# Kernel tuning notes

Hardware: AMD Instinct MI355X
Metric: run time of the kernel (lower is better)

The kernel has to match this reference:

```python
import jax, jax.numpy as jnp
import numpy as np

# Static configuration (matches init_kwargs)
L = 3264          # seq_length
K = 12            # ktc=4 -> K=12
LOCC = 4          # ktc=4 -> Locc=4
S, B, A = 8, 64, 4  # streams (user/port pairs), batch, rx antennas
DELAY_MIN, DELAY_MAX = -10, 10


def _phasor(m):
    # m: integer shifts [S, B] -> exp(1j*2*pi*m*n/L) as [S, B, L]
    n = jnp.arange(L, dtype=jnp.int32)
    ang = (2.0 * np.pi / L) * ((m[..., None] * n) % L).astype(jnp.float32)
    return jax.lax.complex(jnp.cos(ang), jnp.sin(ang))


def _linear_interp(h_avg):
    # np.interp with uniform source grid orig[i] = (LOCC-1)/2 + i*LOCC, clamped at ends.
    # h_avg: [S, B, A, R] complex, R = L // LOCC -> [S, B, A, L]
    R = L // LOCC
    new = jnp.arange(L, dtype=jnp.float32)
    t = jnp.clip((new - (LOCC - 1) / 2.0) / LOCC, 0.0, float(R - 1))
    i0 = jnp.floor(t).astype(jnp.int32)
    i1 = jnp.minimum(i0 + 1, R - 1)
    frac = (t - i0).astype(jnp.float32)
    return h_avg[..., i0] * (1.0 - frac) + h_avg[..., i1] * frac


def reference(ls_real, ls_imag, cyclic_shifts, noise_powers):
    ls = jax.lax.complex(ls_real, ls_imag)                     # [S,B,A,L]
    ideal_peak = ((K - cyclic_shifts) % K) * (L // K)          # [S]

    # Stage 1: IFFT + timing-offset search (torch.no_grad in original)
    h_time = jnp.fft.ifft(ls, axis=-1)
    power = jax.lax.stop_gradient(jnp.sum(jnp.abs(h_time) ** 2, axis=2))  # [S,B,L]
    offs = jnp.arange(DELAY_MIN, DELAY_MAX + 1, dtype=jnp.int32)          # [21]
    cand_idx = (ideal_peak[:, None] + offs[None, :]) % L                   # [S,21]
    cand_idx = jnp.broadcast_to(cand_idx[:, None, :], (S, B, offs.shape[0]))
    cand_pow = jnp.take_along_axis(power, cand_idx, axis=-1)               # [S,B,21]
    t_off = offs[jnp.argmax(cand_pow, axis=-1)]                            # [S,B]
    m = t_off + ideal_peak[:, None]                                        # [S,B]
    ph_m = _phasor(m)        # [S,B,L]
    ph_T = _phasor(t_off)    # [S,B,L]

    # Stage 2: phasor shift, OCC demux, interpolation (inside no_grad in original)
    h_shift = ls * ph_m[:, :, None, :]
    h_avg = h_shift.reshape(S, B, A, L // LOCC, LOCC).mean(-1)             # [S,B,A,L/4]
    h_interp = jax.lax.stop_gradient(_linear_interp(h_avg))                # [S,B,A,L]

    # Stage 3: global residual against stream (0,0)'s LS estimate
    total_recon = jnp.sum(h_interp * jnp.conj(ph_m)[:, :, None, :], axis=0)  # [B,A,L]
    residual = ls[0] - total_recon                                           # [B,A,L]

    # Stage 4: apply residual, MMSE (identity: mmse_module=None), timing recovery
    h_wr = h_interp + residual[None, :, :, None, :].squeeze(3) if False else h_interp + residual[None] * ph_m[:, :, None, :]
    final = h_wr * jnp.conj(ph_T)[:, :, None, :]                             # [S,B,A,L]
    return jnp.stack([final.real, final.imag]).astype(jnp.float32)          # [2,S,B,A,L]


def setup_inputs() -> dict:
    key = jax.random.key(0)
    k1, k2, k3, k4 = jax.random.split(key, 4)
    return {
        "ls_real": jax.random.normal(k1, (S, B, A, L), dtype=jnp.float32),
        "ls_imag": jax.random.normal(k2, (S, B, A, L), dtype=jnp.float32),
        "cyclic_shifts": jax.random.randint(k3, (S,), 0, K, dtype=jnp.int32),
        "noise_powers": jax.random.uniform(k4, (B,), dtype=jnp.float32),
    }
```

## Files before the change

kernel.cpp:

```cpp
#include <hip/hip_runtime.h>

namespace {

constexpr int L = 3264;
constexpr int K = 12;
constexpr int S = 8;
constexpr int B = 64;
constexpr int A = 4;
constexpr int R = 816;
constexpr int NOFF = 21;
constexpr int PEAK_STEP = L / K;
constexpr float TWO_PI = 6.28318530717958647692f;
constexpr float CINV = TWO_PI / (float)L;
constexpr int NCHUNK = (L + 255) / 256;

__device__ __forceinline__ float2 cmul(float2 a, float2 b) {
    return make_float2(a.x * b.x - a.y * b.y, a.x * b.y + a.y * b.x);
}

__device__ __forceinline__ float rdl(float v, int d) {
    return __uint_as_float(__builtin_amdgcn_readlane(__float_as_uint(v), d));
}

__global__ __launch_bounds__(256)
void k_tables(const int* __restrict__ cs, float2* __restrict__ phT,
              float2* __restrict__ phI, float2* __restrict__ tw)
{
    const int g = blockIdx.x * 256 + threadIdx.x;
    if (g < NOFF * L) {
        const int t = g / L, l = g - t * L;
        int j = ((t - 10) * l) % L; if (j < 0) j += L;
        float sv, cv; __sincosf(CINV * (float)j, &sv, &cv);
        phT[g] = make_float2(cv, sv);
    } else if (g < (NOFF + S) * L) {
        const int q = g - NOFF * L;
        const int s = q / L, l = q - s * L;
        const int ideal = ((K - cs[s]) % K) * PEAK_STEP;
        const int j = (ideal * l) % L;
        float sv, cv; __sincosf(CINV * (float)j, &sv, &cv);
        phI[q] = make_float2(cv, sv);
    } else if (g < (NOFF + S + 1) * L) {
        const int j = g - (NOFF + S) * L;
        float sv, cv; __sincosf(CINV * (float)j, &sv, &cv);
        tw[j] = make_float2(cv, sv);
    }
}

__global__ __launch_bounds__(512)
void k_dft(const float* __restrict__ lsr, const float* __restrict__ lsi,
           const int* __restrict__ cs,
           const float2* __restrict__ phT, const float2* __restrict__ phI,
           const float2* __restrict__ tw, float* __restrict__ pow_out)
{
    __shared__ float2 red[8][11];

    const int row = blockIdx.x;
    const int sb = row >> 2;
    const int a = row & 3;
    const int s = sb >> 6;
    const int tid = threadIdx.x;
    const int lane = tid & 63;
    const int w = tid >> 6;
    const int gl = tid & 255;
    const int grp = tid >> 8;
    const int d0 = grp ? 10 : 0;

    const int ideal = ((K - cs[s]) % K) * PEAK_STEP;
    int idx0 = ideal - 10; if (idx0 < 0) idx0 += L;

    const float2 w0 = cmul(phI[s * L + gl], phT[d0 * L + gl]);
    const float2 lv = tw[gl];

    {
    }
    int bidx = idx0 + d0 + (lane < 11 ? lane : 10);
    if (bidx >= L) bidx -= L;
    const int js = (256 * bidx) % L;
    const float2 sv = tw[js];
    float str_[11], sti_[11];
    #pragma unroll
    for (int d = 0; d < 11; ++d) {
        str_[d] = rdl(sv.x, d);
        sti_[d] = rdl(sv.y, d);
    }

    float pwr[11], pwi[11], ar[11], ai[11];
    {
        float cr = w0.x, ci = w0.y;
        pwr[0] = cr; pwi[0] = ci;
        #pragma unroll
        for (int d = 1; d < 11; ++d) {
            const float nr = cr * lv.x - ci * lv.y;
            ci = cr * lv.y + ci * lv.x;
            cr = nr;
            pwr[d] = cr; pwi[d] = ci;
        }
    }
    #pragma unroll
    for (int d = 0; d < 11; ++d) { ar[d] = 0.f; ai[d] = 0.f; }

    const float* __restrict__ pr  = lsr + (size_t)row * L;
    const float* __restrict__ pi_ = lsi + (size_t)row * L;

    for (int it = 0; it < 12; ++it) {
        const float xr = pr[gl + (it << 8)];
        const float xi = pi_[gl + (it << 8)];
        #pragma unroll
        for (int d = 0; d < 11; ++d) {
            ar[d] += xr * pwr[d] - xi * pwi[d];
            ai[d] += xr * pwi[d] + xi * pwr[d];
            const float nr = pwr[d] * str_[d] - pwi[d] * sti_[d];
            pwi[d] = pwr[d] * sti_[d] + pwi[d] * str_[d];
            pwr[d] = nr;
        }
    }
    if (gl < 192) {
        const float xr = pr[gl + 3072];
        const float xi = pi_[gl + 3072];
        #pragma unroll
        for (int d = 0; d < 11; ++d) {
            ar[d] += xr * pwr[d] - xi * pwi[d];
            ai[d] += xr * pwi[d] + xi * pwr[d];
        }
    }

    #pragma unroll
    for (int d = 0; d < 11; ++d) {
        float r = ar[d], im = ai[d];
        #pragma unroll
        for (int o = 32; o > 0; o >>= 1) {
            r  += __shfl_xor(r, o);
            im += __shfl_xor(im, o);
        }
        if (lane == 0) red[w][d] = make_float2(r, im);
    }
    __syncthreads();

    if (tid < NOFF) {
        const int d = tid;
        const int g = (d < 10) ? 0 : 1;
        const int dl = d - g * 10;
        float rr = 0.f, ii = 0.f;
        #pragma unroll
        for (int q = 0; q < 4; ++q) {
            rr += red[4 * g + q][dl].x;
            ii += red[4 * g + q][dl].y;
        }
        pow_out[sb * (NOFF * A) + d * A + a] = rr * rr + ii * ii;
    }
}

__global__ __launch_bounds__(64)
void k_argmax(const float* __restrict__ pow_in, int* __restrict__ toff_out)
{
    const int sb = blockIdx.x;
    const int lane = threadIdx.x;

    float pw = -1.f;
    if (lane < NOFF) {
        const float4 p4 = *(const float4*)(pow_in + sb * (NOFF * A) + lane * A);
        pw = p4.x + p4.y + p4.z + p4.w;
    }
    float mx = pw;
    #pragma unroll
    for (int o = 32; o > 0; o >>= 1) mx = fmaxf(mx, __shfl_xor(mx, o));
    const unsigned long long msk = __ballot(pw == mx);
    const int argd = __ffsll(msk) - 1;
    if (lane == 0) toff_out[sb] = argd - 10;
}

__device__ __forceinline__ float2 havg_entry(
    const float* __restrict__ lsr, const float* __restrict__ lsi,
    const float2* __restrict__ phT, const float2* __restrict__ phI,
    int s, int b, int a, int tf, int i, float2 emp)
{
    const size_t base = ((size_t)(s * B + b) * A + a) * L + 4 * i;
    const float4 xr = *(const float4*)(lsr + base);
    const float4 xi = *(const float4*)(lsi + base);
    const float2 w2 = cmul(phI[s * L + 4 * i], phT[tf * L + 4 * i]);
    float wr = w2.x, wi = w2.y;
    float are, aim, nr;
    are  = xr.x * wr - xi.x * wi;  aim  = xr.x * wi + xi.x * wr;
    nr = wr * emp.x - wi * emp.y;  wi = wr * emp.y + wi * emp.x;  wr = nr;
    are += xr.y * wr - xi.y * wi;  aim += xr.y * wi + xi.y * wr;
    nr = wr * emp.x - wi * emp.y;  wi = wr * emp.y + wi * emp.x;  wr = nr;
    are += xr.z * wr - xi.z * wi;  aim += xr.z * wi + xi.z * wr;
    nr = wr * emp.x - wi * emp.y;  wi = wr * emp.y + wi * emp.x;  wr = nr;
    are += xr.w * wr - xi.w * wi;  aim += xr.w * wi + xi.w * wr;
    return make_float2(are * 0.25f, aim * 0.25f);
}

__global__ __launch_bounds__(256)
void k_final(const float* __restrict__ lsr, const float* __restrict__ lsi,
             const int* __restrict__ toff_arr,
             const float2* __restrict__ phT, const float2* __restrict__ phI,
             float* __restrict__ out)
{
    const int bid = blockIdx.x;
    const int chunk = bid % NCHUNK;
    const int ba = bid / NCHUNK;
    const int b = ba >> 2;
    const int a = ba & 3;
    const int l = chunk * 256 + (int)threadIdx.x;
    if (l >= L) return;

    float t2 = ((float)l - 1.5f) * 0.25f;
    t2 = fminf(fmaxf(t2, 0.0f), (float)(R - 1));
    const int i0 = (int)t2;
    const int i1 = min(i0 + 1, R - 1);
    const float frac = t2 - (float)i0;

    float hire[S], hiim[S], pmre[S], pmim[S], ptre[S], ptim[S];
    float rre = 0.f, rim = 0.f;

    #pragma unroll
    for (int s = 0; s < S; ++s) {
        const int tf = toff_arr[s * B + b] + 10;
        const float2 emp = cmul(phI[s * L + 1], phT[tf * L + 1]);
        const float2 h0 = havg_entry(lsr, lsi, phT, phI, s, b, a, tf, i0, emp);
        const float2 h1 = havg_entry(lsr, lsi, phT, phI, s, b, a, tf, i1, emp);
        const float hr = h0.x * (1.f - frac) + h1.x * frac;
        const float hi = h0.y * (1.f - frac) + h1.y * frac;
        const float2 pt = phT[tf * L + l];
        const float2 wm = cmul(phI[s * L + l], pt);
        hire[s] = hr; hiim[s] = hi;
        pmre[s] = wm.x; pmim[s] = wm.y;
        ptre[s] = pt.x; ptim[s] = pt.y;
        rre += hr * wm.x + hi * wm.y;
        rim += hi * wm.x - hr * wm.y;
    }

    const size_t off0 = ((size_t)(b * A + a)) * L + l;
    const float resre = lsr[off0] - rre;
    const float resim = lsi[off0] - rim;

    #pragma unroll
    for (int s = 0; s < S; ++s) {
        const float wre = hire[s] + resre * pmre[s] - resim * pmim[s];
        const float wim = hiim[s] + resre * pmim[s] + resim * pmre[s];
        const float fre = wre * ptre[s] + wim * ptim[s];
        const float fim = wim * ptre[s] - wre * ptim[s];
        const size_t o = (((size_t)(s * B + b)) * A + a) * L + l;
        out[o] = fre;
        out[(size_t)S * B * A * L + o] = fim;
    }
}

}

extern "C" void kernel_launch(void* const* d_in, const int* in_sizes, int n_in,
                              void* d_out, int out_size, void* d_ws, size_t ws_size,
                              hipStream_t stream) {
    (void)in_sizes; (void)n_in; (void)out_size; (void)ws_size;
    const float* lsr = (const float*)d_in[0];
    const float* lsi = (const float*)d_in[1];
    const int*   cs  = (const int*)d_in[2];

    int* toff = (int*)d_ws;
    float2* phT  = (float2*)((char*)d_ws + 4096);
    float2* phI  = (float2*)((char*)d_ws + 552448);
    float2* tw   = (float2*)((char*)d_ws + 761344);
    float*  powb = (float*)((char*)d_ws + 787456);

    const int ntab = ((NOFF + S + 1) * L + 255) / 256;
    k_tables<<<ntab, 256, 0, stream>>>(cs, phT, phI, tw);
    k_dft   <<<S * B * A, 512, 0, stream>>>(lsr, lsi, cs, phT, phI, tw, powb);
    k_argmax<<<S * B, 64, 0, stream>>>(powb, toff);
    k_final <<<B * A * NCHUNK, 256, 0, stream>>>(lsr, lsi, toff, phT, phI,
                                                 (float*)d_out);
}
```

Measured before the change: 181.1 us.

## Precompute OCC-averaged channel in separate kernel and pack DFT rotations as vectors

Adds a k_havg kernel that computes each averaged channel entry once and writes it to workspace. k_final then reads two precomputed values per stream instead of recomputing each average from raw float4 loads and phasor products. In the old code every output thread did this recomputation, and neighbouring outputs share averages, so much of that work was redundant. The DFT inner loop is also rewritten with two-wide float vectors, which may let the compiler emit packed FMA instructions. In exchange there is an extra kernel launch plus a workspace write and read of the averages.

```diff
diff --git a/kernel.cpp b/kernel.cpp
--- a/kernel.cpp
+++ b/kernel.cpp
@@ -13,6 +13,8 @@
 constexpr float TWO_PI = 6.28318530717958647692f;
 constexpr float CINV = TWO_PI / (float)L;
 constexpr int NCHUNK = (L + 255) / 256;
+
+typedef float v2f __attribute__((ext_vector_type(2)));
 
 __device__ __forceinline__ float2 cmul(float2 a, float2 b) {
     return make_float2(a.x * b.x - a.y * b.y, a.x * b.y + a.y * b.x);
@@ -71,33 +73,31 @@
     const float2 w0 = cmul(phI[s * L + gl], phT[d0 * L + gl]);
     const float2 lv = tw[gl];
 
-    {
-    }
     int bidx = idx0 + d0 + (lane < 11 ? lane : 10);
     if (bidx >= L) bidx -= L;
     const int js = (256 * bidx) % L;
     const float2 sv = tw[js];
-    float str_[11], sti_[11];
+    float sr_[11], si_[11];
     #pragma unroll
     for (int d = 0; d < 11; ++d) {
-        str_[d] = rdl(sv.x, d);
-        sti_[d] = rdl(sv.y, d);
-    }
-
-    float pwr[11], pwi[11], ar[11], ai[11];
+        sr_[d] = rdl(sv.x, d);
+        si_[d] = rdl(sv.y, d);
+    }
+
+    v2f nw[11], nc[11], acc[11];
     {
         float cr = w0.x, ci = w0.y;
-        pwr[0] = cr; pwi[0] = ci;
-        #pragma unroll
-        for (int d = 1; d < 11; ++d) {
+        #pragma unroll
+        for (int d = 0; d < 11; ++d) {
+            nw[d] = (v2f){cr, ci};
+            nc[d] = (v2f){-ci, cr};
             const float nr = cr * lv.x - ci * lv.y;
             ci = cr * lv.y + ci * lv.x;
             cr = nr;
-            pwr[d] = cr; pwi[d] = ci;
-        }
-    }
-    #pragma unroll
-    for (int d = 0; d < 11; ++d) { ar[d] = 0.f; ai[d] = 0.f; }
+        }
+    }
+    #pragma unroll
+    for (int d = 0; d < 11; ++d) acc[d] = (v2f){0.f, 0.f};
 
     const float* __restrict__ pr  = lsr + (size_t)row * L;
     const float* __restrict__ pi_ = lsi + (size_t)row * L;
@@ -107,26 +107,23 @@
         const float xi = pi_[gl + (it << 8)];
         #pragma unroll
         for (int d = 0; d < 11; ++d) {
-            ar[d] += xr * pwr[d] - xi * pwi[d];
-            ai[d] += xr * pwi[d] + xi * pwr[d];
-            const float nr = pwr[d] * str_[d] - pwi[d] * sti_[d];
-            pwi[d] = pwr[d] * sti_[d] + pwi[d] * str_[d];
-            pwr[d] = nr;
+            acc[d] += nw[d] * xr + nc[d] * xi;
+            const v2f t = nw[d] * sr_[d] + nc[d] * si_[d];
+            nc[d] = nc[d] * sr_[d] - nw[d] * si_[d];
+            nw[d] = t;
         }
     }
     if (gl < 192) {
         const float xr = pr[gl + 3072];
         const float xi = pi_[gl + 3072];
         #pragma unroll
-        for (int d = 0; d < 11; ++d) {
-            ar[d] += xr * pwr[d] - xi * pwi[d];
-            ai[d] += xr * pwi[d] + xi * pwr[d];
-        }
+        for (int d = 0; d < 11; ++d)
+            acc[d] += nw[d] * xr + nc[d] * xi;
     }
 
     #pragma unroll
     for (int d = 0; d < 11; ++d) {
-        float r = ar[d], im = ai[d];
+        float r = acc[d].x, im = acc[d].y;
         #pragma unroll
         for (int o = 32; o > 0; o >>= 1) {
             r  += __shfl_xor(r, o);
@@ -169,39 +166,60 @@
     if (lane == 0) toff_out[sb] = argd - 10;
 }
 
-__device__ __forceinline__ float2 havg_entry(
-    const float* __restrict__ lsr, const float* __restrict__ lsi,
-    const float2* __restrict__ phT, const float2* __restrict__ phI,
-    int s, int b, int a, int tf, int i, float2 emp)
-{
-    const size_t base = ((size_t)(s * B + b) * A + a) * L + 4 * i;
-    const float4 xr = *(const float4*)(lsr + base);
-    const float4 xi = *(const float4*)(lsi + base);
-    const float2 w2 = cmul(phI[s * L + 4 * i], phT[tf * L + 4 * i]);
-    float wr = w2.x, wi = w2.y;
-    float are, aim, nr;
-    are  = xr.x * wr - xi.x * wi;  aim  = xr.x * wi + xi.x * wr;
-    nr = wr * emp.x - wi * emp.y;  wi = wr * emp.y + wi * emp.x;  wr = nr;
-    are += xr.y * wr - xi.y * wi;  aim += xr.y * wi + xi.y * wr;
-    nr = wr * emp.x - wi * emp.y;  wi = wr * emp.y + wi * emp.x;  wr = nr;
-    are += xr.z * wr - xi.z * wi;  aim += xr.z * wi + xi.z * wr;
-    nr = wr * emp.x - wi * emp.y;  wi = wr * emp.y + wi * emp.x;  wr = nr;
-    are += xr.w * wr - xi.w * wi;  aim += xr.w * wi + xi.w * wr;
-    return make_float2(are * 0.25f, aim * 0.25f);
+__global__ __launch_bounds__(256)
+void k_havg(const float* __restrict__ lsr, const float* __restrict__ lsi,
+            const int* __restrict__ toff_arr,
+            const float2* __restrict__ phT, const float2* __restrict__ phI,
+            float2* __restrict__ havg)
+{
+    const int row = blockIdx.x;
+    const int sb = row >> 2;
+    const int s = sb >> 6;
+    const int tid = threadIdx.x;
+
+    const int tf = toff_arr[sb] + 10;
+    const float2 emp = cmul(phI[s * L + 1], phT[tf * L + 1]);
+
+    const float4* __restrict__ qr4 = (const float4*)(lsr + (size_t)row * L);
+    const float4* __restrict__ qi4 = (const float4*)(lsi + (size_t)row * L);
+    float2* __restrict__ dst = havg + (size_t)row * R;
+
+    for (int i = tid; i < R; i += 256) {
+        const float2 w2 = cmul(phI[s * L + 4 * i], phT[tf * L + 4 * i]);
+        const float4 xr = qr4[i];
+        const float4 xi = qi4[i];
+        float wr = w2.x, wi = w2.y;
+        float are, aim, nr;
+        are  = xr.x * wr - xi.x * wi;  aim  = xr.x * wi + xi.x * wr;
+        nr = wr * emp.x - wi * emp.y;  wi = wr * emp.y + wi * emp.x;  wr = nr;
+        are += xr.y * wr - xi.y * wi;  aim += xr.y * wi + xi.y * wr;
+        nr = wr * emp.x - wi * emp.y;  wi = wr * emp.y + wi * emp.x;  wr = nr;
+        are += xr.z * wr - xi.z * wi;  aim += xr.z * wi + xi.z * wr;
+        nr = wr * emp.x - wi * emp.y;  wi = wr * emp.y + wi * emp.x;  wr = nr;
+        are += xr.w * wr - xi.w * wi;  aim += xr.w * wi + xi.w * wr;
+        dst[i] = make_float2(are * 0.25f, aim * 0.25f);
+    }
 }
 
 __global__ __launch_bounds__(256)
 void k_final(const float* __restrict__ lsr, const float* __restrict__ lsi,
-             const int* __restrict__ toff_arr,
+             const int* __restrict__ toff_arr, const float2* __restrict__ havg,
              const float2* __restrict__ phT, const float2* __restrict__ phI,
              float* __restrict__ out)
 {
+    __shared__ int tfs[S];
+
     const int bid = blockIdx.x;
     const int chunk = bid % NCHUNK;
     const int ba = bid / NCHUNK;
     const int b = ba >> 2;
     const int a = ba & 3;
-    const int l = chunk * 256 + (int)threadIdx.x;
+    const int tid = threadIdx.x;
+
+    if (tid < S) tfs[tid] = toff_arr[tid * B + b] + 10;
+    __syncthreads();
+
+    const int l = chunk * 256 + tid;
     if (l >= L) return;
 
     float t2 = ((float)l - 1.5f) * 0.25f;
@@ -215,10 +233,10 @@
 
     #pragma unroll
     for (int s = 0; s < S; ++s) {
-        const int tf = toff_arr[s * B + b] + 10;
-        const float2 emp = cmul(phI[s * L + 1], phT[tf * L + 1]);
-        const float2 h0 = havg_entry(lsr, lsi, phT, phI, s, b, a, tf, i0, emp);
-        const float2 h1 = havg_entry(lsr, lsi, phT, phI, s, b, a, tf, i1, emp);
+        const int tf = tfs[s];
+        const size_t hb = ((size_t)(s * B + b) * A + a) * R;
+        const float2 h0 = havg[hb + i0];
+        const float2 h1 = havg[hb + i1];
         const float hr = h0.x * (1.f - frac) + h1.x * frac;
         const float hi = h0.y * (1.f - frac) + h1.y * frac;
         const float2 pt = phT[tf * L + l];
@@ -261,11 +279,13 @@
     float2* phI  = (float2*)((char*)d_ws + 552448);
     float2* tw   = (float2*)((char*)d_ws + 761344);
     float*  powb = (float*)((char*)d_ws + 787456);
+    float2* havg = (float2*)((char*)d_ws + 962560);
 
     const int ntab = ((NOFF + S + 1) * L + 255) / 256;
     k_tables<<<ntab, 256, 0, stream>>>(cs, phT, phI, tw);
     k_dft   <<<S * B * A, 512, 0, stream>>>(lsr, lsi, cs, phT, phI, tw, powb);
     k_argmax<<<S * B, 64, 0, stream>>>(powb, toff);
-    k_final <<<B * A * NCHUNK, 256, 0, stream>>>(lsr, lsi, toff, phT, phI,
+    k_havg  <<<S * B * A, 256, 0, stream>>>(lsr, lsi, toff, phT, phI, havg);
+    k_final <<<B * A * NCHUNK, 256, 0, stream>>>(lsr, lsi, toff, havg, phT, phI,
                                                  (float*)d_out);
 }
```

Result: slower. 186.5 us (+3.0%).

## Restructure DFT kernel with register-held inputs and fuse argmax into final kernel

Applied to the files above, without the earlier changes.

The DFT power kernel now runs with 256 threads; each thread holds its samples as float4 registers and loops over the 21 delay candidates, advancing the twiddles by recurrence instead of keeping 11 accumulators per thread. The separate argmax kernel is removed and its work moves into the final kernel. That kernel also computes each needed OCC-averaged entry once into shared memory per chunk, rather than recomputing it twice per output sample. This saves one launch and the redundant global loads and math, at the cost of a shuffle reduction per delay and a longer twiddle recurrence chain that may lose float accuracy.

```diff
diff --git a/kernel.cpp b/kernel.cpp
--- a/kernel.cpp
+++ b/kernel.cpp
@@ -13,13 +13,10 @@
 constexpr float TWO_PI = 6.28318530717958647692f;
 constexpr float CINV = TWO_PI / (float)L;
 constexpr int NCHUNK = (L + 255) / 256;
+constexpr int HS_MAX = 66;
 
 __device__ __forceinline__ float2 cmul(float2 a, float2 b) {
     return make_float2(a.x * b.x - a.y * b.y, a.x * b.y + a.y * b.x);
-}
-
-__device__ __forceinline__ float rdl(float v, int d) {
-    return __uint_as_float(__builtin_amdgcn_readlane(__float_as_uint(v), d));
 }
 
 __global__ __launch_bounds__(256)
@@ -46,13 +43,13 @@
     }
 }
 
-__global__ __launch_bounds__(512)
+__global__ __launch_bounds__(256, 6)
 void k_dft(const float* __restrict__ lsr, const float* __restrict__ lsi,
            const int* __restrict__ cs,
            const float2* __restrict__ phT, const float2* __restrict__ phI,
            const float2* __restrict__ tw, float* __restrict__ pow_out)
 {
-    __shared__ float2 red[8][11];
+    __shared__ float2 red[4][NOFF];
 
     const int row = blockIdx.x;
     const int sb = row >> 2;
@@ -61,147 +58,132 @@
     const int tid = threadIdx.x;
     const int lane = tid & 63;
     const int w = tid >> 6;
-    const int gl = tid & 255;
-    const int grp = tid >> 8;
-    const int d0 = grp ? 10 : 0;
 
     const int ideal = ((K - cs[s]) % K) * PEAK_STEP;
     int idx0 = ideal - 10; if (idx0 < 0) idx0 += L;
 
-    const float2 w0 = cmul(phI[s * L + gl], phT[d0 * L + gl]);
-    const float2 lv = tw[gl];
-
-    {
-    }
-    int bidx = idx0 + d0 + (lane < 11 ? lane : 10);
-    if (bidx >= L) bidx -= L;
-    const int js = (256 * bidx) % L;
-    const float2 sv = tw[js];
-    float str_[11], sti_[11];
-    #pragma unroll
-    for (int d = 0; d < 11; ++d) {
-        str_[d] = rdl(sv.x, d);
-        sti_[d] = rdl(sv.y, d);
-    }
-
-    float pwr[11], pwi[11], ar[11], ai[11];
-    {
-        float cr = w0.x, ci = w0.y;
-        pwr[0] = cr; pwi[0] = ci;
-        #pragma unroll
-        for (int d = 1; d < 11; ++d) {
-            const float nr = cr * lv.x - ci * lv.y;
-            ci = cr * lv.y + ci * lv.x;
-            cr = nr;
-            pwr[d] = cr; pwi[d] = ci;
+    const float4* __restrict__ pr4 = (const float4*)(lsr + (size_t)row * L);
+    const float4* __restrict__ pi4 = (const float4*)(lsi + (size_t)row * L);
+    float4 xr[4], xi[4];
+    xr[0] = pr4[tid];       xi[0] = pi4[tid];
+    xr[1] = pr4[tid + 256]; xi[1] = pi4[tid + 256];
+    xr[2] = pr4[tid + 512]; xi[2] = pi4[tid + 512];
+    xr[3] = make_float4(0.f, 0.f, 0.f, 0.f);
+    xi[3] = make_float4(0.f, 0.f, 0.f, 0.f);
+    if (tid < 48) { xr[3] = pr4[tid + 768]; xi[3] = pi4[tid + 768]; }
+
+    const float2 e1 = tw[1];
+    const float2 E1 = tw[1024];
+    float2 e = tw[idx0];
+    float2 E = tw[(1024 * idx0) % L];
+    const float2 t4 = tw[4 * tid];
+    float2 wb = cmul(phI[s * L + 4 * tid], phT[4 * tid]);
+
+    for (int d = 0; d < NOFF; ++d) {
+        float ac_r = 0.f, ac_i = 0.f;
+        float2 w2 = wb;
+        #pragma unroll
+        for (int g = 0; g < 4; ++g) {
+            float2 u = w2;
+            ac_r += xr[g].x * u.x - xi[g].x * u.y;
+            ac_i += xr[g].x * u.y + xi[g].x * u.x;
+            u = cmul(u, e);
+            ac_r += xr[g].y * u.x - xi[g].y * u.y;
+            ac_i += xr[g].y * u.y + xi[g].y * u.x;
+            u = cmul(u, e);
+            ac_r += xr[g].z * u.x - xi[g].z * u.y;
+            ac_i += xr[g].z * u.y + xi[g].z * u.x;
+            u = cmul(u, e);
+            ac_r += xr[g].w * u.x - xi[g].w * u.y;
+            ac_i += xr[g].w * u.y + xi[g].w * u.x;
+            if (g < 3) w2 = cmul(w2, E);
         }
-    }
-    #pragma unroll
-    for (int d = 0; d < 11; ++d) { ar[d] = 0.f; ai[d] = 0.f; }
-
-    const float* __restrict__ pr  = lsr + (size_t)row * L;
-    const float* __restrict__ pi_ = lsi + (size_t)row * L;
-
-    for (int it = 0; it < 12; ++it) {
-        const float xr = pr[gl + (it << 8)];
-        const float xi = pi_[gl + (it << 8)];
-        #pragma unroll
-        for (int d = 0; d < 11; ++d) {
-            ar[d] += xr * pwr[d] - xi * pwi[d];
-            ai[d] += xr * pwi[d] + xi * pwr[d];
-            const float nr = pwr[d] * str_[d] - pwi[d] * sti_[d];
-            pwi[d] = pwr[d] * sti_[d] + pwi[d] * str_[d];
-            pwr[d] = nr;
+        #pragma unroll
+        for (int o = 32; o > 0; o >>= 1) {
+            ac_r += __shfl_xor(ac_r, o);
+            ac_i += __shfl_xor(ac_i, o);
         }
-    }
-    if (gl < 192) {
-        const float xr = pr[gl + 3072];
-        const float xi = pi_[gl + 3072];
-        #pragma unroll
-        for (int d = 0; d < 11; ++d) {
-            ar[d] += xr * pwr[d] - xi * pwi[d];
-            ai[d] += xr * pwi[d] + xi * pwr[d];
-        }
-    }
-
-    #pragma unroll
-    for (int d = 0; d < 11; ++d) {
-        float r = ar[d], im = ai[d];
-        #pragma unroll
-        for (int o = 32; o > 0; o >>= 1) {
-            r  += __shfl_xor(r, o);
-            im += __shfl_xor(im, o);
-        }
-        if (lane == 0) red[w][d] = make_float2(r, im);
+        if (lane == 0) red[w][d] = make_float2(ac_r, ac_i);
+        wb = cmul(wb, t4);
+        e  = cmul(e,  e1);
+        E  = cmul(E,  E1);
     }
     __syncthreads();
 
     if (tid < NOFF) {
-        const int d = tid;
-        const int g = (d < 10) ? 0 : 1;
-        const int dl = d - g * 10;
         float rr = 0.f, ii = 0.f;
         #pragma unroll
-        for (int q = 0; q < 4; ++q) {
-            rr += red[4 * g + q][dl].x;
-            ii += red[4 * g + q][dl].y;
-        }
-        pow_out[sb * (NOFF * A) + d * A + a] = rr * rr + ii * ii;
-    }
-}
-
-__global__ __launch_bounds__(64)
-void k_argmax(const float* __restrict__ pow_in, int* __restrict__ toff_out)
-{
-    const int sb = blockIdx.x;
-    const int lane = threadIdx.x;
-
-    float pw = -1.f;
-    if (lane < NOFF) {
-        const float4 p4 = *(const float4*)(pow_in + sb * (NOFF * A) + lane * A);
-        pw = p4.x + p4.y + p4.z + p4.w;
-    }
-    float mx = pw;
-    #pragma unroll
-    for (int o = 32; o > 0; o >>= 1) mx = fmaxf(mx, __shfl_xor(mx, o));
-    const unsigned long long msk = __ballot(pw == mx);
-    const int argd = __ffsll(msk) - 1;
-    if (lane == 0) toff_out[sb] = argd - 10;
-}
-
-__device__ __forceinline__ float2 havg_entry(
-    const float* __restrict__ lsr, const float* __restrict__ lsi,
-    const float2* __restrict__ phT, const float2* __restrict__ phI,
-    int s, int b, int a, int tf, int i, float2 emp)
-{
-    const size_t base = ((size_t)(s * B + b) * A + a) * L + 4 * i;
-    const float4 xr = *(const float4*)(lsr + base);
-    const float4 xi = *(const float4*)(lsi + base);
-    const float2 w2 = cmul(phI[s * L + 4 * i], phT[tf * L + 4 * i]);
-    float wr = w2.x, wi = w2.y;
-    float are, aim, nr;
-    are  = xr.x * wr - xi.x * wi;  aim  = xr.x * wi + xi.x * wr;
-    nr = wr * emp.x - wi * emp.y;  wi = wr * emp.y + wi * emp.x;  wr = nr;
-    are += xr.y * wr - xi.y * wi;  aim += xr.y * wi + xi.y * wr;
-    nr = wr * emp.x - wi * emp.y;  wi = wr * emp.y + wi * emp.x;  wr = nr;
-    are += xr.z * wr - xi.z * wi;  aim += xr.z * wi + xi.z * wr;
-    nr = wr * emp.x - wi * emp.y;  wi = wr * emp.y + wi * emp.x;  wr = nr;
-    are += xr.w * wr - xi.w * wi;  aim += xr.w * wi + xi.w * wr;
-    return make_float2(are * 0.25f, aim * 0.25f);
+        for (int q = 0; q < 4; ++q) { rr += red[q][tid].x; ii += red[q][tid].y; }
+        pow_out[sb * (NOFF * A) + tid * A + a] = rr * rr + ii * ii;
+    }
 }
 
 __global__ __launch_bounds__(256)
-void k_final(const float* __restrict__ lsr, const float* __restrict__ lsi,
-             const int* __restrict__ toff_arr,
+void k_fused(const float* __restrict__ lsr, const float* __restrict__ lsi,
+             const float* __restrict__ powb,
              const float2* __restrict__ phT, const float2* __restrict__ phI,
              float* __restrict__ out)
 {
+    __shared__ float pw[S][NOFF];
+    __shared__ float2 hs[S][HS_MAX];
+    __shared__ float2 emps[S];
+    __shared__ int tfs[S];
+
     const int bid = blockIdx.x;
     const int chunk = bid % NCHUNK;
     const int ba = bid / NCHUNK;
     const int b = ba >> 2;
     const int a = ba & 3;
-    const int l = chunk * 256 + (int)threadIdx.x;
+    const int tid = threadIdx.x;
+
+    if (tid < S * NOFF) {
+        const int s = tid / NOFF;
+        const int d = tid - s * NOFF;
+        const float4 p4 = ((const float4*)powb)[(s * B + b) * NOFF + d];
+        pw[s][d] = p4.x + p4.y + p4.z + p4.w;
+    }
+    __syncthreads();
+
+    if (tid < S) {
+        float best = pw[tid][0]; int bd = 0;
+        #pragma unroll
+        for (int d = 1; d < NOFF; ++d)
+            if (pw[tid][d] > best) { best = pw[tid][d]; bd = d; }
+        tfs[tid] = bd;
+        emps[tid] = cmul(phI[tid * L + 1], phT[bd * L + 1]);
+    }
+    __syncthreads();
+
+    const int imin = max(0, chunk * 64 - 1);
+    const int imax = min(R - 1, chunk * 64 + 64);
+    const int cnt = imax - imin + 1;
+
+    for (int t = tid; t < S * HS_MAX; t += 256) {
+        const int s = t / HS_MAX;
+        const int ii = t - s * HS_MAX;
+        if (ii < cnt) {
+            const int i = imin + ii;
+            const int tf = tfs[s];
+            const float2 emp = emps[s];
+            const size_t base = ((size_t)(s * B + b) * A + a) * L + 4 * i;
+            const float4 xr = *(const float4*)(lsr + base);
+            const float4 xi = *(const float4*)(lsi + base);
+            const float2 w2 = cmul(phI[s * L + 4 * i], phT[tf * L + 4 * i]);
+            float wr = w2.x, wi = w2.y;
+            float are, aim, nr;
+            are  = xr.x * wr - xi.x * wi;  aim  = xr.x * wi + xi.x * wr;
+            nr = wr * emp.x - wi * emp.y;  wi = wr * emp.y + wi * emp.x;  wr = nr;
+            are += xr.y * wr - xi.y * wi;  aim += xr.y * wi + xi.y * wr;
+            nr = wr * emp.x - wi * emp.y;  wi = wr * emp.y + wi * emp.x;  wr = nr;
+            are += xr.z * wr - xi.z * wi;  aim += xr.z * wi + xi.z * wr;
+            nr = wr * emp.x - wi * emp.y;  wi = wr * emp.y + wi * emp.x;  wr = nr;
+            are += xr.w * wr - xi.w * wi;  aim += xr.w * wi + xi.w * wr;
+            hs[s][ii] = make_float2(are * 0.25f, aim * 0.25f);
+        }
+    }
+    __syncthreads();
+
+    const int l = chunk * 256 + tid;
     if (l >= L) return;
 
     float t2 = ((float)l - 1.5f) * 0.25f;
@@ -215,10 +197,9 @@
 
     #pragma unroll
     for (int s = 0; s < S; ++s) {
-        const int tf = toff_arr[s * B + b] + 10;
-        const float2 emp = cmul(phI[s * L + 1], phT[tf * L + 1]);
-        const float2 h0 = havg_entry(lsr, lsi, phT, phI, s, b, a, tf, i0, emp);
-        const float2 h1 = havg_entry(lsr, lsi, phT, phI, s, b, a, tf, i1, emp);
+        const int tf = tfs[s];
+        const float2 h0 = hs[s][i0 - imin];
+        const float2 h1 = hs[s][i1 - imin];
         const float hr = h0.x * (1.f - frac) + h1.x * frac;
         const float hi = h0.y * (1.f - frac) + h1.y * frac;
         const float2 pt = phT[tf * L + l];
@@ -256,7 +237,6 @@
     const float* lsi = (const float*)d_in[1];
     const int*   cs  = (const int*)d_in[2];
 
-    int* toff = (int*)d_ws;
     float2* phT  = (float2*)((char*)d_ws + 4096);
     float2* phI  = (float2*)((char*)d_ws + 552448);
     float2* tw   = (float2*)((char*)d_ws + 761344);
@@ -264,8 +244,7 @@
 
     const int ntab = ((NOFF + S + 1) * L + 255) / 256;
     k_tables<<<ntab, 256, 0, stream>>>(cs, phT, phI, tw);
-    k_dft   <<<S * B * A, 512, 0, stream>>>(lsr, lsi, cs, phT, phI, tw, powb);
-    k_argmax<<<S * B, 64, 0, stream>>>(powb, toff);
-    k_final <<<B * A * NCHUNK, 256, 0, stream>>>(lsr, lsi, toff, phT, phI,
+    k_dft   <<<S * B * A, 256, 0, stream>>>(lsr, lsi, cs, phT, phI, tw, powb);
+    k_fused <<<B * A * NCHUNK, 256, 0, stream>>>(lsr, lsi, powb, phT, phI,
                                                  (float*)d_out);
 }
```

Measured after the change: 177.7 us. No clear change (-1.9%).
